# Optimization experiments

Hardware: AMD Instinct MI355X
Metric: run time of the kernel (lower is better)

## Reference

```python
import jax, jax.numpy as jnp
import numpy as np

N = 100000
E = 1600000
IN_F = 128
HIDDEN = 128
HEADS = 2
N_CLASSES = 40
NEG_SLOPE = 0.2
BN_EPS = 1e-5


def setup_inputs() -> dict:
    key = jax.random.key(0)
    ks = jax.random.split(key, 12)
    c1 = HIDDEN // HEADS  # 64
    c2 = N_CLASSES        # 40 per head, concat=False
    inp = {
        "x": jax.random.normal(ks[0], (N, IN_F), dtype=jnp.float32),
        "edge_index": jax.random.randint(ks[1], (2, E), 0, N, dtype=jnp.int32),
        # layer 1 GATConv params
        "W1": jax.random.normal(ks[2], (IN_F, HEADS * c1), dtype=jnp.float32) * 0.05,
        "att_src1": jax.random.normal(ks[3], (HEADS, c1), dtype=jnp.float32) * 0.05,
        "att_dst1": jax.random.normal(ks[4], (HEADS, c1), dtype=jnp.float32) * 0.05,
        "b1": jnp.zeros((HEADS * c1,), dtype=jnp.float32),
        # BatchNorm params
        "gamma": jnp.ones((HIDDEN,), dtype=jnp.float32),
        "beta": jnp.zeros((HIDDEN,), dtype=jnp.float32),
        # layer 2 GATConv params (concat=False)
        "W2": jax.random.normal(ks[5], (HIDDEN, HEADS * c2), dtype=jnp.float32) * 0.05,
        "att_src2": jax.random.normal(ks[6], (HEADS, c2), dtype=jnp.float32) * 0.05,
        "att_dst2": jax.random.normal(ks[7], (HEADS, c2), dtype=jnp.float32) * 0.05,
        "b2": jnp.zeros((c2,), dtype=jnp.float32),
    }
    return inp


def gat_conv(x, src, dst, W, att_src, att_dst, bias, heads, concat):
    n = x.shape[0]
    h = (x @ W).reshape(n, heads, -1)             # [N, H, C]
    a_src = jnp.sum(h * att_src[None], axis=-1)   # [N, H]
    a_dst = jnp.sum(h * att_dst[None], axis=-1)   # [N, H]
    alpha = jax.nn.leaky_relu(a_src[src] + a_dst[dst], NEG_SLOPE)  # [E, H]
    # numerically-stable segment softmax over edges grouped by dst
    amax = jax.ops.segment_max(alpha, dst, num_segments=n)
    e = jnp.exp(alpha - amax[dst])
    denom = jax.ops.segment_sum(e, dst, num_segments=n)
    w = e / denom[dst]                            # [E, H]
    msg = h[src] * w[:, :, None]                  # [E, H, C]
    out = jax.ops.segment_sum(msg, dst, num_segments=n)  # [N, H, C]
    if concat:
        out = out.reshape(n, -1)
    else:
        out = out.mean(axis=1)
    return out + bias


def batch_norm(x, gamma, beta):
    mean = x.mean(axis=0)
    var = x.var(axis=0)
    return (x - mean) * jax.lax.rsqrt(var + BN_EPS) * gamma + beta


def reference(x, edge_index, W1, att_src1, att_dst1, b1, gamma, beta,
              W2, att_src2, att_dst2, b2):
    n = x.shape[0]
    # PyG GATConv default: add self-loops
    loops = jnp.arange(n, dtype=edge_index.dtype)
    src = jnp.concatenate([edge_index[0], loops])
    dst = jnp.concatenate([edge_index[1], loops])
    h = gat_conv(x, src, dst, W1, att_src1, att_dst1, b1, HEADS, concat=True)
    h = batch_norm(h, gamma, beta)
    h = gat_conv(h, src, dst, W2, att_src2, att_dst2, b2, HEADS, concat=False)
    return jax.nn.log_softmax(h, axis=1)
```

## Files before the change

kernel.cpp:

```cpp
#include <hip/hip_runtime.h>
#include <hip/hip_bf16.h>
#include <hip/hip_fp16.h>
#include <stdint.h>

#define N_NODES 100000
#define N_EDGES 1600000
#define ET (N_EDGES + N_NODES)
#define HID 128
#define C2 40
#define F2 80
#define NEG 0.2f
#define BN_EPS 1e-5f
#define NBUCK 391
#define BCAP 6144
#define NBB 640
#define EPB ((ET + NBB - 1) / NBB)
#define CH2 256

typedef __hip_bfloat16 bf16;
typedef __attribute__((ext_vector_type(8))) short s8v;
typedef __attribute__((ext_vector_type(4))) float f4v;
typedef __attribute__((ext_vector_type(4))) unsigned int u4v;
typedef __attribute__((ext_vector_type(2))) unsigned int u2v;

__device__ __forceinline__ float b2f(bf16 v){ return __bfloat162float(v); }
__device__ __forceinline__ float rdf(const void* p, size_t i, int isb){
    return isb ? b2f(((const bf16*)p)[i]) : ((const float*)p)[i];
}
__device__ __forceinline__ unsigned short f2bb(float v){
    bf16 h = __float2bfloat16(v);
    return *(unsigned short*)&h;
}
__device__ __forceinline__ uint32_t pack2(float a, float b){
    return (uint32_t)f2bb(a) | ((uint32_t)f2bb(b) << 16);
}
__device__ __forceinline__ uint32_t packh2(float a, float b){
    return (uint32_t)__half_as_ushort(__float2half(a))
         | ((uint32_t)__half_as_ushort(__float2half(b)) << 16);
}
__device__ __forceinline__ float lo16(uint32_t u){ return __uint_as_float(u << 16); }
__device__ __forceinline__ float hi16(uint32_t u){ return __uint_as_float(u & 0xFFFF0000u); }
__device__ __forceinline__ float hcvt(uint32_t w, int sh){
    return __half2float(__ushort_as_half((unsigned short)((w >> sh) & 0xFFFFu)));
}

__global__ __launch_bounds__(256) void k_init(
    const uint32_t* __restrict__ w1bits, int* __restrict__ flag,
    int* __restrict__ gcur, float* __restrict__ stats)
{
    __shared__ int cnt;
    int t = threadIdx.x;
    if (t == 0) cnt = 0;
    __syncthreads();
    uint32_t b = w1bits[t];
    float lo = __uint_as_float((b & 0xFFFFu) << 16);
    float a = fabsf(lo);
    if (a > 1e-8f && a < 1.0f) atomicAdd(&cnt, 1);
    for (int i = t; i < NBUCK; i += 256) gcur[i] = 0;
    stats[t] = 0.f;
    __syncthreads();
    if (t == 0) *flag = (cnt >= 192) ? 1 : 0;
}

__global__ __launch_bounds__(256) void k_gemm1(
    const void* __restrict__ x, const void* __restrict__ W1,
    const void* __restrict__ attS, const void* __restrict__ attD,
    const int* __restrict__ flag, unsigned short* __restrict__ h1,
    float* __restrict__ aS, float* __restrict__ aD)
{
    __shared__ __attribute__((aligned(16))) unsigned short wT[128*132];
    const int isb = *flag;
    const int tid = threadIdx.x;
    if (isb) {
        const unsigned short* w = (const unsigned short*)W1;
        for (int idx = tid; idx < 128*128; idx += 256){
            int k = idx >> 7, n = idx & 127;
            wT[n*132 + k] = w[idx];
        }
    } else {
        const float* w = (const float*)W1;
        for (int idx = tid; idx < 128*128; idx += 256){
            int k = idx >> 7, n = idx & 127;
            wT[n*132 + k] = f2bb(w[idx]);
        }
    }
    __syncthreads();

    const int w4 = tid >> 6, lane = tid & 63, quad = lane >> 4, l16 = lane & 15;
    const int rowbase = blockIdx.x*32 + (w4 >> 1)*16;
    const int colbase = (w4 & 1)*64;
    const int head = w4 & 1;

    s8v bfr[4][4];
    float asv[4], adv[4];
    #pragma unroll
    for (int ct = 0; ct < 4; ct++){
        int n = colbase + ct*16 + l16;
        asv[ct] = rdf(attS, n, isb);
        adv[ct] = rdf(attD, n, isb);
        #pragma unroll
        for (int s = 0; s < 4; s++){
            int k0 = s*32 + quad*8;
            const unsigned short* p = &wT[n*132 + k0];
            u2v a = *(const u2v*)p, b = *(const u2v*)(p+4);
            union { u4v u; s8v s; } cv; cv.u = (u4v){a[0],a[1],b[0],b[1]};
            bfr[ct][s] = cv.s;
        }
    }

    f4v acc[4];
    #pragma unroll
    for (int ct = 0; ct < 4; ct++) acc[ct] = (f4v){0.f,0.f,0.f,0.f};

    const int m = rowbase + l16;
    #pragma unroll
    for (int s = 0; s < 4; s++){
        int k0 = s*32 + quad*8;
        s8v af;
        if (isb){
            union { u4v u; s8v s; } cv;
            cv.u = *(const u4v*)((const unsigned short*)x + (size_t)m*128 + k0);
            af = cv.s;
        } else {
            const float* xp = (const float*)x + (size_t)m*128 + k0;
            f4v f0 = *(const f4v*)xp, f1 = *(const f4v*)(xp+4);
            union { u4v u; s8v s; } cv;
            cv.u = (u4v){pack2(f0[0],f0[1]), pack2(f0[2],f0[3]),
                         pack2(f1[0],f1[1]), pack2(f1[2],f1[3])};
            af = cv.s;
        }
        #pragma unroll
        for (int ct = 0; ct < 4; ct++)
            acc[ct] = __builtin_amdgcn_mfma_f32_16x16x32_bf16(af, bfr[ct][s], acc[ct], 0,0,0);
    }

    #pragma unroll
    for (int ct = 0; ct < 4; ct++){
        int col = colbase + ct*16 + l16;
        #pragma unroll
        for (int r = 0; r < 4; r++){
            int row = rowbase + quad*4 + r;
            h1[(size_t)row*128 + col] = f2bb(acc[ct][r]);
        }
    }

    #pragma unroll
    for (int r = 0; r < 4; r++){
        float vs = 0.f, vd = 0.f;
        #pragma unroll
        for (int ct = 0; ct < 4; ct++){ vs += acc[ct][r]*asv[ct]; vd += acc[ct][r]*adv[ct]; }
        #pragma unroll
        for (int o = 1; o < 16; o <<= 1){
            vs += __shfl_xor(vs, o, 64);
            vd += __shfl_xor(vd, o, 64);
        }
        if (l16 == 0){
            int row = rowbase + quad*4 + r;
            aS[row*2 + head] = vs;
            aD[row*2 + head] = vd;
        }
    }
}

__global__ __launch_bounds__(256) void k_bin(
    const int* __restrict__ esrc, const int* __restrict__ edst,
    int* __restrict__ gcur, uint32_t* __restrict__ staging)
{
    __shared__ int cnt[NBUCK];
    __shared__ int bb[NBUCK];
    const int t = threadIdx.x;
    for (int i = t; i < NBUCK; i += 256) cnt[i] = 0;
    __syncthreads();
    const int e0 = blockIdx.x * EPB;
    const int e1 = (e0 + EPB < ET) ? e0 + EPB : ET;
    for (int e = e0 + t; e < e1; e += 256){
        int d = (e < N_EDGES) ? edst[e] : e - N_EDGES;
        atomicAdd(&cnt[d >> 8], 1);
    }
    __syncthreads();
    const int bofs = (int)(blockIdx.x % NBUCK);
    for (int i = t; i < NBUCK; i += 256){
        int bkt = i + bofs; if (bkt >= NBUCK) bkt -= NBUCK;
        int c = cnt[bkt];
        bb[bkt] = c ? atomicAdd(&gcur[bkt], c) : 0;
        cnt[bkt] = 0;
    }
    __syncthreads();
    for (int e = e0 + t; e < e1; e += 256){
        int d, s;
        if (e < N_EDGES){ s = esrc[e]; d = edst[e]; } else { s = d = e - N_EDGES; }
        int b = d >> 8;
        int r = atomicAdd(&cnt[b], 1);
        int p = bb[b] + r;
        if (p < BCAP) staging[(size_t)b*BCAP + p] = ((uint32_t)s << 8) | (uint32_t)(d & 255);
    }
}

__global__ __launch_bounds__(256) void k_sort(
    const int* __restrict__ gcur, const uint32_t* __restrict__ staging,
    int* __restrict__ deg, int* __restrict__ cur, int* __restrict__ eidx)
{
    __shared__ int h[256], sc[256], rk[256];
    __shared__ int lsrc[BCAP];
    const int b = blockIdx.x;
    const int t = threadIdx.x;
    const int base = b * BCAP;
    int cnt = gcur[b];
    if (cnt > BCAP) cnt = BCAP;
    h[t] = 0; rk[t] = 0;
    __syncthreads();
    for (int i = t; i < cnt; i += 256)
        atomicAdd(&h[staging[base + i] & 255u], 1);
    __syncthreads();
    sc[t] = h[t];
    __syncthreads();
    for (int off = 1; off < 256; off <<= 1){
        int v = (t >= off) ? sc[t - off] : 0;
        __syncthreads();
        sc[t] += v;
        __syncthreads();
    }
    int dg = b*256 + t;
    if (dg < N_NODES){
        deg[dg] = h[t];
        cur[dg] = base + sc[t];
    }
    __syncthreads();
    for (int i = t; i < cnt; i += 256){
        uint32_t w = staging[base + i];
        int dl = w & 255u;
        int r = atomicAdd(&rk[dl], 1);
        lsrc[sc[dl] - h[dl] + r] = (int)(w >> 8);
    }
    __syncthreads();
    for (int i = t; i < cnt; i += 256) eidx[base + i] = lsrc[i];
}

__global__ __launch_bounds__(256) void k_agg1(
    const int* __restrict__ cur, const int* __restrict__ deg,
    const int* __restrict__ eidx, const float* __restrict__ aS,
    const float* __restrict__ aD, const uint32_t* __restrict__ h1u,
    uint32_t* __restrict__ out1u)
{
    __shared__ uint2 lse[4][2][CH2 + 4];
    const int wv = threadIdx.x >> 6;
    const int l = threadIdx.x & 63;
    const int half = l >> 5, ll = l & 31;
    const int d = blockIdx.x*8 + wv*2 + half;
    const int c = ll & 15;
    const int g = ll >> 4;
    const uint32_t c16 = (uint32_t)(c*16);
    int end   = cur[d];
    int start = end - deg[d];
    float2 ad = *(const float2*)(aD + d*2);
    const int sh = (c >= 8) ? 16 : 0;
    float den0 = 0.f, den1 = 0.f;
    float acc[8];
    #pragma unroll
    for (int k = 0; k < 8; k++) acc[k] = 0.f;
    const char* hb = (const char*)h1u;

#define G1(P, W) { u4v Gx = *(const u4v*)(hb + ((P).x + c16)); \
    float Wf = (W); \
    acc[0] += Wf*lo16(Gx[0]); acc[1] += Wf*hi16(Gx[0]); \
    acc[2] += Wf*lo16(Gx[1]); acc[3] += Wf*hi16(Gx[1]); \
    acc[4] += Wf*lo16(Gx[2]); acc[5] += Wf*hi16(Gx[2]); \
    acc[6] += Wf*lo16(Gx[3]); acc[7] += Wf*hi16(Gx[3]); }

    for (int c0 = start; c0 < end; c0 += CH2){
        int c1 = (c0 + CH2 < end) ? c0 + CH2 : end;
        int n = c1 - c0;
        for (int j = c0 + ll; j < c1; j += 32){
            int s = eidx[j];
            float2 as = *(const float2*)((const char*)aS + ((uint32_t)s*8u));
            float al0 = as.x + ad.x, al1 = as.y + ad.y;
            al0 = al0 > 0.f ? al0 : NEG*al0;
            al1 = al1 > 0.f ? al1 : NEG*al1;
            float e0 = __expf(al0), e1 = __expf(al1);
            lse[wv][half][j - c0] = make_uint2((uint32_t)s << 8, packh2(e0, e1));
            den0 += e0; den1 += e1;
        }
        int nn = (n + 1) & ~1;
        if (ll < nn - n) lse[wv][half][n + ll] = make_uint2(0u, 0u);
        int i = 0;
        for (; i + 8 <= nn; i += 8){
            uint2 pa = lse[wv][half][i + g];
            uint2 pb = lse[wv][half][i + 2 + g];
            uint2 pc = lse[wv][half][i + 4 + g];
            uint2 pd = lse[wv][half][i + 6 + g];
            G1(pa, hcvt(pa.y, sh));
            G1(pb, hcvt(pb.y, sh));
            G1(pc, hcvt(pc.y, sh));
            G1(pd, hcvt(pd.y, sh));
        }
        for (; i < nn; i += 2){
            uint2 pa = lse[wv][half][i + g];
            G1(pa, hcvt(pa.y, sh));
        }
    }
#undef G1
    #pragma unroll
    for (int o = 1; o < 32; o <<= 1){
        den0 += __shfl_xor(den0, o, 64);
        den1 += __shfl_xor(den1, o, 64);
    }
    #pragma unroll
    for (int k = 0; k < 8; k++)
        acc[k] += __shfl_xor(acc[k], 16, 64);
    float r = 1.f / fmaxf((c < 8) ? den0 : den1, 1e-20f);
    if (ll < 16){
        u4v o;
        #pragma unroll
        for (int q = 0; q < 4; q++) o[q] = pack2(acc[2*q]*r, acc[2*q+1]*r);
        *(u4v*)(out1u + (size_t)d*64 + 4*c) = o;
    }
}

__global__ __launch_bounds__(256) void k_bnstats(
    const uint32_t* __restrict__ out1u, float* __restrict__ stats)
{
    __shared__ float red[4][64][4];
    int fp = threadIdx.x & 63;
    int wv = threadIdx.x >> 6;
    float s0 = 0.f, q0 = 0.f, s1 = 0.f, q1 = 0.f;
    for (int r = blockIdx.x*4 + wv; r < N_NODES; r += 512){
        uint32_t u = out1u[(size_t)r*64 + fp];
        float f0 = lo16(u), f1 = hi16(u);
        s0 += f0; q0 += f0*f0; s1 += f1; q1 += f1*f1;
    }
    red[wv][fp][0] = s0; red[wv][fp][1] = s1;
    red[wv][fp][2] = q0; red[wv][fp][3] = q1;
    __syncthreads();
    if (threadIdx.x < 64){
        int l = threadIdx.x;
        float a0=0.f, a1=0.f, b0=0.f, b1=0.f;
        #pragma unroll
        for (int w = 0; w < 4; w++){
            a0 += red[w][l][0]; a1 += red[w][l][1];
            b0 += red[w][l][2]; b1 += red[w][l][3];
        }
        unsafeAtomicAdd(&stats[2*l],       a0);
        unsafeAtomicAdd(&stats[2*l+1],     a1);
        unsafeAtomicAdd(&stats[128+2*l],   b0);
        unsafeAtomicAdd(&stats[128+2*l+1], b1);
    }
}

__global__ __launch_bounds__(256) void k_gemm2(
    const unsigned short* __restrict__ out1b, const float* __restrict__ stats,
    const void* __restrict__ gamma, const void* __restrict__ beta,
    const void* __restrict__ W2, const void* __restrict__ attS,
    const void* __restrict__ attD, const int* __restrict__ flag,
    unsigned short* __restrict__ h2, float* __restrict__ aS, float* __restrict__ aD)
{
    __shared__ __attribute__((aligned(16))) unsigned short wT[80*132];
    __shared__ float scl[128], shl[128];
    const int isb = *flag;
    const int tid = threadIdx.x;
    for (int idx = tid; idx < 128*80; idx += 256){
        int k = idx / 80, n = idx - k*80;
        wT[n*132 + k] = isb ? ((const unsigned short*)W2)[idx]
                            : f2bb(((const float*)W2)[idx]);
    }
    if (tid < 128){
        float mean = stats[tid] * (1.f / N_NODES);
        float var = fmaxf(stats[128+tid] * (1.f / N_NODES) - mean*mean, 0.f);
        float rs = rsqrtf(var + BN_EPS);
        float sc = rdf(gamma, tid, isb) * rs;
        scl[tid] = sc;
        shl[tid] = rdf(beta, tid, isb) - mean*sc;
    }
    __syncthreads();

    const int w4 = tid >> 6, lane = tid & 63, quad = lane >> 4, l16 = lane & 15;
    const int rowbase = blockIdx.x*64 + w4*16;

    s8v bfr[5][4];
    float asv[5], adv[5];
    #pragma unroll
    for (int ct = 0; ct < 5; ct++){
        int n = ct*16 + l16;
        asv[ct] = rdf(attS, n, isb);
        adv[ct] = rdf(attD, n, isb);
        #pragma unroll
        for (int s = 0; s < 4; s++){
            int k0 = s*32 + quad*8;
            const unsigned short* p = &wT[n*132 + k0];
            u2v a = *(const u2v*)p, b = *(const u2v*)(p+4);
            union { u4v u; s8v s; } cv; cv.u = (u4v){a[0],a[1],b[0],b[1]};
            bfr[ct][s] = cv.s;
        }
    }

    f4v acc[5];
    #pragma unroll
    for (int ct = 0; ct < 5; ct++) acc[ct] = (f4v){0.f,0.f,0.f,0.f};

    int m = rowbase + l16;
    int mc = m < N_NODES ? m : N_NODES - 1;
    #pragma unroll
    for (int s = 0; s < 4; s++){
        int k0 = s*32 + quad*8;
        union { u4v u; s8v s8; } cin;
        cin.u = *(const u4v*)(out1b + (size_t)mc*128 + k0);
        u4v up;
        #pragma unroll
        for (int i = 0; i < 4; i++){
            float f0 = lo16(cin.u[i]), f1 = hi16(cin.u[i]);
            int k = k0 + 2*i;
            up[i] = pack2(f0*scl[k] + shl[k], f1*scl[k+1] + shl[k+1]);
        }
        union { u4v u; s8v s8; } cv; cv.u = up;
        #pragma unroll
        for (int ct = 0; ct < 5; ct++)
            acc[ct] = __builtin_amdgcn_mfma_f32_16x16x32_bf16(cv.s8, bfr[ct][s], acc[ct], 0,0,0);
    }

    #pragma unroll
    for (int ct = 0; ct < 5; ct++){
        int col = ct*16 + l16;
        #pragma unroll
        for (int r = 0; r < 4; r++){
            int row = rowbase + quad*4 + r;
            if (row < N_NODES) h2[(size_t)row*80 + col] = f2bb(acc[ct][r]);
        }
    }

    #pragma unroll
    for (int r = 0; r < 4; r++){
        float vs0 = 0.f, vs1 = 0.f, vd0 = 0.f, vd1 = 0.f;
        #pragma unroll
        for (int ct = 0; ct < 5; ct++){
            int col = ct*16 + l16;
            float ps = acc[ct][r]*asv[ct], pd = acc[ct][r]*adv[ct];
            if (col < 40){ vs0 += ps; vd0 += pd; } else { vs1 += ps; vd1 += pd; }
        }
        #pragma unroll
        for (int o = 1; o < 16; o <<= 1){
            vs0 += __shfl_xor(vs0, o, 64); vs1 += __shfl_xor(vs1, o, 64);
            vd0 += __shfl_xor(vd0, o, 64); vd1 += __shfl_xor(vd1, o, 64);
        }
        if (l16 == 0){
            int row = rowbase + quad*4 + r;
            if (row < N_NODES){
                aS[row*2 + 0] = vs0; aS[row*2 + 1] = vs1;
                aD[row*2 + 0] = vd0; aD[row*2 + 1] = vd1;
            }
        }
    }
}

__global__ __launch_bounds__(256) void k_agg2(
    const int* __restrict__ cur, const int* __restrict__ deg,
    const int* __restrict__ eidx, const float* __restrict__ aS,
    const float* __restrict__ aD, const uint32_t* __restrict__ h2u,
    const void* __restrict__ b2v, const int* __restrict__ flag,
    void* __restrict__ out)
{
    __shared__ uint2 lse[4][2][CH2 + 4];
    const int wv = threadIdx.x >> 6;
    const int l = threadIdx.x & 63;
    const int half = l >> 5, ll = l & 31;
    const int d = blockIdx.x*8 + wv*2 + half;
    const int isb = *flag;
    const int c = ll % 10;
    const int g = ll / 10;
    const bool act = ll < 30;
    const int gq = act ? g : 0;
    const uint32_t c16 = (uint32_t)(c*16);
    int end   = cur[d];
    int start = end - deg[d];
    float2 ad = *(const float2*)(aD + d*2);
    const int sh = (c >= 5) ? 16 : 0;
    float den0 = 0.f, den1 = 0.f;
    float acc[8];
    #pragma unroll
    for (int k = 0; k < 8; k++) acc[k] = 0.f;
    const char* hb = (const char*)h2u;

#define G2(P, W) { u4v Gx = *(const u4v*)(hb + ((P).x + c16)); \
    float Wf = (W); \
    acc[0] += Wf*lo16(Gx[0]); acc[1] += Wf*hi16(Gx[0]); \
    acc[2] += Wf*lo16(Gx[1]); acc[3] += Wf*hi16(Gx[1]); \
    acc[4] += Wf*lo16(Gx[2]); acc[5] += Wf*hi16(Gx[2]); \
    acc[6] += Wf*lo16(Gx[3]); acc[7] += Wf*hi16(Gx[3]); }

    for (int c0 = start; c0 < end; c0 += CH2){
        int c1 = (c0 + CH2 < end) ? c0 + CH2 : end;
        int n = c1 - c0;
        for (int j = c0 + ll; j < c1; j += 32){
            int s = eidx[j];
            float2 as = *(const float2*)((const char*)aS + ((uint32_t)s*8u));
            float al0 = as.x + ad.x, al1 = as.y + ad.y;
            al0 = al0 > 0.f ? al0 : NEG*al0;
            al1 = al1 > 0.f ? al1 : NEG*al1;
            float e0 = __expf(al0), e1 = __expf(al1);
            lse[wv][half][j - c0] = make_uint2((uint32_t)s * 160u, packh2(e0, e1));
            den0 += e0; den1 += e1;
        }
        int nn = ((n + 2) / 3) * 3;
        if (ll < nn - n) lse[wv][half][n + ll] = make_uint2(0u, 0u);
        int i = 0;
        for (; i + 9 <= nn; i += 9){
            uint2 pa = lse[wv][half][i + gq];
            uint2 pb = lse[wv][half][i + 3 + gq];
            uint2 pc = lse[wv][half][i + 6 + gq];
            G2(pa, act ? hcvt(pa.y, sh) : 0.f);
            G2(pb, act ? hcvt(pb.y, sh) : 0.f);
            G2(pc, act ? hcvt(pc.y, sh) : 0.f);
        }
        for (; i < nn; i += 3){
            uint2 pa = lse[wv][half][i + gq];
            G2(pa, act ? hcvt(pa.y, sh) : 0.f);
        }
    }
#undef G2
    #pragma unroll
    for (int o = 1; o < 32; o <<= 1){
        den0 += __shfl_xor(den0, o, 64);
        den1 += __shfl_xor(den1, o, 64);
    }
    #pragma unroll
    for (int k = 0; k < 8; k++)
        acc[k] += __shfl(acc[k], l + 10, 64) + __shfl(acc[k], l + 20, 64);
    float r = 1.f / fmaxf((c < 5) ? den0 : den1, 1e-20f);
    #pragma unroll
    for (int k = 0; k < 8; k++) acc[k] *= r;

    int lb = (ll < 5) ? ll : 0;
    float v[8];
    float mx = -1e30f;
    #pragma unroll
    for (int k = 0; k < 8; k++){
        float t = __shfl(acc[k], l + 5, 64);
        v[k] = 0.5f*(acc[k] + t) + rdf(b2v, 8*lb + k, isb);
        mx = fmaxf(mx, v[k]);
    }
    if (ll >= 5) mx = -1e30f;
    mx = fmaxf(mx, __shfl_xor(mx, 1, 64));
    mx = fmaxf(mx, __shfl_xor(mx, 2, 64));
    mx = fmaxf(mx, __shfl_xor(mx, 4, 64));
    float ex = 0.f;
    if (ll < 5){
        #pragma unroll
        for (int k = 0; k < 8; k++) ex += __expf(v[k] - mx);
    }
    ex += __shfl_xor(ex, 1, 64);
    ex += __shfl_xor(ex, 2, 64);
    ex += __shfl_xor(ex, 4, 64);
    float lsf = __logf(ex);
    if (ll < 5){
        if (isb){
            u4v o;
            #pragma unroll
            for (int q = 0; q < 4; q++)
                o[q] = pack2(v[2*q] - mx - lsf, v[2*q+1] - mx - lsf);
            *(u4v*)((uint32_t*)out + (size_t)d*20 + 4*ll) = o;
        } else {
            float4 o0, o1;
            o0.x = v[0]-mx-lsf; o0.y = v[1]-mx-lsf; o0.z = v[2]-mx-lsf; o0.w = v[3]-mx-lsf;
            o1.x = v[4]-mx-lsf; o1.y = v[5]-mx-lsf; o1.z = v[6]-mx-lsf; o1.w = v[7]-mx-lsf;
            ((float4*)out)[(size_t)d*10 + 2*ll]     = o0;
            ((float4*)out)[(size_t)d*10 + 2*ll + 1] = o1;
        }
    }
}

extern "C" void kernel_launch(void* const* d_in, const int* in_sizes, int n_in,
                              void* d_out, int out_size, void* d_ws, size_t ws_size,
                              hipStream_t stream)
{
    const void* x    = d_in[0];
    const int*  ei   = (const int*)d_in[1];
    const void* W1   = d_in[2];
    const void* as1  = d_in[3];
    const void* ad1  = d_in[4];
    const void* gamma = d_in[6];
    const void* beta  = d_in[7];
    const void* W2   = d_in[8];
    const void* as2  = d_in[9];
    const void* ad2  = d_in[10];
    const void* b2v  = d_in[11];
    const int* esrc = ei;
    const int* edst = ei + N_EDGES;

    char* ws = (char*)d_ws;
    size_t off = 0;
    auto alloc = [&](size_t bytes) {
        void* p = ws + off;
        off += (bytes + 255) & ~(size_t)255;
        return p;
    };
    int*   flag  = (int*)alloc(256);
    float* stats = (float*)alloc(sizeof(float)*256);
    int*   gcur  = (int*)alloc(sizeof(int)*NBUCK);
    float* aS1   = (float*)alloc(sizeof(float)*N_NODES*2);
    float* aD1   = (float*)alloc(sizeof(float)*N_NODES*2);
    float* aS2   = (float*)alloc(sizeof(float)*N_NODES*2);
    float* aD2   = (float*)alloc(sizeof(float)*N_NODES*2);
    int*   deg   = (int*)alloc(sizeof(int)*N_NODES);
    int*   cur   = (int*)alloc(sizeof(int)*N_NODES);
    uint32_t* staging = (uint32_t*)alloc(sizeof(uint32_t)*(size_t)NBUCK*BCAP);
    int*   eidx  = (int*)alloc(sizeof(int)*(size_t)NBUCK*BCAP);
    unsigned short* h1  = (unsigned short*)alloc(2*(size_t)N_NODES*HID);
    unsigned short* out1 = (unsigned short*)alloc(2*(size_t)N_NODES*HID);
    unsigned short* h2  = h1;

    k_init<<<1, 256, 0, stream>>>((const uint32_t*)W1, flag, gcur, stats);
    k_gemm1<<<3125, 256, 0, stream>>>(x, W1, as1, ad1, flag, h1, aS1, aD1);
    k_bin<<<NBB, 256, 0, stream>>>(esrc, edst, gcur, staging);
    k_sort<<<NBUCK, 256, 0, stream>>>(gcur, staging, deg, cur, eidx);
    k_agg1<<<12500, 256, 0, stream>>>(cur, deg, eidx, aS1, aD1,
                                      (const uint32_t*)h1, (uint32_t*)out1);
    k_bnstats<<<128, 256, 0, stream>>>((const uint32_t*)out1, stats);
    k_gemm2<<<1563, 256, 0, stream>>>(out1, stats, gamma, beta, W2, as2, ad2,
                                      flag, h2, aS2, aD2);
    k_agg2<<<12500, 256, 0, stream>>>(cur, deg, eidx, aS2, aD2,
                                      (const uint32_t*)h2, b2v, flag, d_out);
}
```

Measured before the change: 412.7 us.

## Split layer-1 aggregation per head across blocks with fp32 edge weights

The layer-1 aggregation kernel now assigns each head of a destination node to a separate 32-lane group, doubling the grid so that head 0 and head 1 are processed by different blocks. Each lane-group now gathers 128-byte head slices (8 lanes × 16B) for four edges at once instead of 256-byte rows for two. Edge weights are stored as fp32 rather than packed half2, which removes the half conversion. This is meant to raise parallelism and memory-level concurrency for the gathers. The cost is that the edge index and attention scores are read twice and the exp is computed once per head rather than for both heads together.

```diff
diff --git a/kernel.cpp b/kernel.cpp
--- a/kernel.cpp
+++ b/kernel.cpp
@@ -246,22 +246,25 @@
     const int wv = threadIdx.x >> 6;
     const int l = threadIdx.x & 63;
     const int half = l >> 5, ll = l & 31;
-    const int d = blockIdx.x*8 + wv*2 + half;
-    const int c = ll & 15;
-    const int g = ll >> 4;
+    const int bx = blockIdx.x;
+    const int grp = bx >> 3, xp = bx & 7;
+    const int h = xp >> 2, sub = xp & 3;
+    const int d = grp*32 + sub*8 + wv*2 + half;
+    const int c = ll & 7;
+    const int g = ll >> 3;
     const uint32_t c16 = (uint32_t)(c*16);
+    const uint32_t hofs = (uint32_t)h << 7;
     int end   = cur[d];
     int start = end - deg[d];
-    float2 ad = *(const float2*)(aD + d*2);
-    const int sh = (c >= 8) ? 16 : 0;
-    float den0 = 0.f, den1 = 0.f;
+    float adh = aD[d*2 + h];
+    float den = 0.f;
     float acc[8];
     #pragma unroll
     for (int k = 0; k < 8; k++) acc[k] = 0.f;
     const char* hb = (const char*)h1u;
 
-#define G1(P, W) { u4v Gx = *(const u4v*)(hb + ((P).x + c16)); \
-    float Wf = (W); \
+#define G1(P) { u4v Gx = *(const u4v*)(hb + ((P).x + c16)); \
+    float Wf = __uint_as_float((P).y); \
     acc[0] += Wf*lo16(Gx[0]); acc[1] += Wf*hi16(Gx[0]); \
     acc[2] += Wf*lo16(Gx[1]); acc[3] += Wf*hi16(Gx[1]); \
     acc[4] += Wf*lo16(Gx[2]); acc[5] += Wf*hi16(Gx[2]); \
@@ -272,47 +275,44 @@
         int n = c1 - c0;
         for (int j = c0 + ll; j < c1; j += 32){
             int s = eidx[j];
-            float2 as = *(const float2*)((const char*)aS + ((uint32_t)s*8u));
-            float al0 = as.x + ad.x, al1 = as.y + ad.y;
-            al0 = al0 > 0.f ? al0 : NEG*al0;
-            al1 = al1 > 0.f ? al1 : NEG*al1;
-            float e0 = __expf(al0), e1 = __expf(al1);
-            lse[wv][half][j - c0] = make_uint2((uint32_t)s << 8, packh2(e0, e1));
-            den0 += e0; den1 += e1;
-        }
-        int nn = (n + 1) & ~1;
-        if (ll < nn - n) lse[wv][half][n + ll] = make_uint2(0u, 0u);
+            float as = ((const float*)aS)[(size_t)s*2 + h];
+            float al = as + adh;
+            al = al > 0.f ? al : NEG*al;
+            float e = __expf(al);
+            lse[wv][half][j - c0] = make_uint2(((uint32_t)s << 8) + hofs,
+                                               __float_as_uint(e));
+            den += e;
+        }
+        int nn = (n + 3) & ~3;
+        if (ll < nn - n) lse[wv][half][n + ll] = make_uint2(hofs, 0u);
         int i = 0;
-        for (; i + 8 <= nn; i += 8){
-            uint2 pa = lse[wv][half][i + g];
-            uint2 pb = lse[wv][half][i + 2 + g];
-            uint2 pc = lse[wv][half][i + 4 + g];
-            uint2 pd = lse[wv][half][i + 6 + g];
-            G1(pa, hcvt(pa.y, sh));
-            G1(pb, hcvt(pb.y, sh));
-            G1(pc, hcvt(pc.y, sh));
-            G1(pd, hcvt(pd.y, sh));
-        }
-        for (; i < nn; i += 2){
-            uint2 pa = lse[wv][half][i + g];
-            G1(pa, hcvt(pa.y, sh));
+        for (; i + 16 <= nn; i += 16){
+            uint2 q0 = lse[wv][half][i + g];
+            uint2 q1 = lse[wv][half][i + 4 + g];
+            uint2 q2 = lse[wv][half][i + 8 + g];
+            uint2 q3 = lse[wv][half][i + 12 + g];
+            G1(q0); G1(q1); G1(q2); G1(q3);
+        }
+        for (; i < nn; i += 4){
+            uint2 q0 = lse[wv][half][i + g];
+            G1(q0);
         }
     }
 #undef G1
     #pragma unroll
-    for (int o = 1; o < 32; o <<= 1){
-        den0 += __shfl_xor(den0, o, 64);
-        den1 += __shfl_xor(den1, o, 64);
-    }
-    #pragma unroll
-    for (int k = 0; k < 8; k++)
+    for (int o = 1; o < 32; o <<= 1)
+        den += __shfl_xor(den, o, 64);
+    #pragma unroll
+    for (int k = 0; k < 8; k++){
+        acc[k] += __shfl_xor(acc[k], 8, 64);
         acc[k] += __shfl_xor(acc[k], 16, 64);
-    float r = 1.f / fmaxf((c < 8) ? den0 : den1, 1e-20f);
-    if (ll < 16){
+    }
+    float r = 1.f / fmaxf(den, 1e-20f);
+    if (ll < 8){
         u4v o;
         #pragma unroll
         for (int q = 0; q < 4; q++) o[q] = pack2(acc[2*q]*r, acc[2*q+1]*r);
-        *(u4v*)(out1u + (size_t)d*64 + 4*c) = o;
+        *(u4v*)(out1u + (size_t)d*64 + h*32 + 4*c) = o;
     }
 }
 
@@ -610,7 +610,7 @@
     k_gemm1<<<3125, 256, 0, stream>>>(x, W1, as1, ad1, flag, h1, aS1, aD1);
     k_bin<<<NBB, 256, 0, stream>>>(esrc, edst, gcur, staging);
     k_sort<<<NBUCK, 256, 0, stream>>>(gcur, staging, deg, cur, eidx);
-    k_agg1<<<12500, 256, 0, stream>>>(cur, deg, eidx, aS1, aD1,
+    k_agg1<<<25000, 256, 0, stream>>>(cur, deg, eidx, aS1, aD1,
                                       (const uint32_t*)h1, (uint32_t*)out1);
     k_bnstats<<<128, 256, 0, stream>>>((const uint32_t*)out1, stats);
     k_gemm2<<<1563, 256, 0, stream>>>(out1, stats, gamma, beta, W2, as2, ad2,
```

Result: no change. 411.0 us (-0.4%).

## Precompute layer-1 edge weights and denominators in sort; split agg1 by feature slice

Applied to the files above, without the earlier changes.

The layer-1 attention exponentials and per-node softmax denominators now come out of the sort kernel, packed with the source index into 32-bit words (17-bit src, 15-bit fp16 weight without its sign bit), one buffer per head. agg1 then runs 8x more blocks, each handling a 32-byte feature slice of one head and reading precomputed weights without shared-memory staging. The aim is to drop redundant exp/gather work and raise parallelism in the gather. In exchange, each edge word is read several times, the denominator loop in sort runs serially per thread, and packing the source index into 17 bits limits node ids to 131072.

```diff
diff --git a/kernel.cpp b/kernel.cpp
--- a/kernel.cpp
+++ b/kernel.cpp
@@ -42,6 +42,9 @@
 __device__ __forceinline__ float hi16(uint32_t u){ return __uint_as_float(u & 0xFFFF0000u); }
 __device__ __forceinline__ float hcvt(uint32_t w, int sh){
     return __half2float(__ushort_as_half((unsigned short)((w >> sh) & 0xFFFFu)));
+}
+__device__ __forceinline__ float w15f(uint32_t w){
+    return __half2float(__ushort_as_half((unsigned short)(w & 0x7FFFu)));
 }
 
 __global__ __launch_bounds__(256) void k_init(
@@ -197,8 +200,10 @@
 }
 
 __global__ __launch_bounds__(256) void k_sort(
-    const int* __restrict__ gcur, const uint32_t* __restrict__ staging,
-    int* __restrict__ deg, int* __restrict__ cur, int* __restrict__ eidx)
+    const int* __restrict__ gcur, uint32_t* stg ,
+    const float* __restrict__ aS, const float* __restrict__ aD,
+    int* __restrict__ deg, int* __restrict__ cur,
+    uint32_t* __restrict__ wb1, float* __restrict__ den)
 {
     __shared__ int h[256], sc[256], rk[256];
     __shared__ int lsrc[BCAP];
@@ -210,7 +215,7 @@
     h[t] = 0; rk[t] = 0;
     __syncthreads();
     for (int i = t; i < cnt; i += 256)
-        atomicAdd(&h[staging[base + i] & 255u], 1);
+        atomicAdd(&h[stg[base + i] & 255u], 1);
     __syncthreads();
     sc[t] = h[t];
     __syncthreads();
@@ -227,92 +232,107 @@
     }
     __syncthreads();
     for (int i = t; i < cnt; i += 256){
-        uint32_t w = staging[base + i];
+        uint32_t w = stg[base + i];
         int dl = w & 255u;
         int r = atomicAdd(&rk[dl], 1);
         lsrc[sc[dl] - h[dl] + r] = (int)(w >> 8);
     }
     __syncthreads();
-    for (int i = t; i < cnt; i += 256) eidx[base + i] = lsrc[i];
+    if (dg < N_NODES){
+        int myDeg = h[t];
+        int myStart = sc[t] - h[t];
+        float2 adv = *(const float2*)(aD + (size_t)dg*2);
+        float den0 = 0.f, den1 = 0.f;
+        for (int i = 0; i < myDeg; i++){
+            int s = lsrc[myStart + i];
+            float2 as = *(const float2*)(aS + (size_t)s*2);
+            float al0 = as.x + adv.x, al1 = as.y + adv.y;
+            al0 = al0 > 0.f ? al0 : NEG*al0;
+            al1 = al1 > 0.f ? al1 : NEG*al1;
+            float e0 = __expf(al0), e1 = __expf(al1);
+            den0 += e0; den1 += e1;
+            uint32_t sb = (uint32_t)s << 15;
+            uint32_t p0 = (uint32_t)__half_as_ushort(__float2half(e0)) & 0x7FFFu;
+            uint32_t p1 = (uint32_t)__half_as_ushort(__float2half(e1)) & 0x7FFFu;
+            stg[base + myStart + i] = sb | p0;
+            wb1[base + myStart + i] = sb | p1;
+        }
+        den[(size_t)dg*2]     = den0;
+        den[(size_t)dg*2 + 1] = den1;
+    }
 }
 
 __global__ __launch_bounds__(256) void k_agg1(
     const int* __restrict__ cur, const int* __restrict__ deg,
-    const int* __restrict__ eidx, const float* __restrict__ aS,
-    const float* __restrict__ aD, const uint32_t* __restrict__ h1u,
+    const uint32_t* __restrict__ wb0, const uint32_t* __restrict__ wb1,
+    const float* __restrict__ den, const uint32_t* __restrict__ h1u,
     uint32_t* __restrict__ out1u)
 {
-    __shared__ uint2 lse[4][2][CH2 + 4];
+    const int bx = blockIdx.x;
+    const int k = bx & 7;
+    const int grp = bx >> 3;
+    const int h = k >> 2;
+    const uint32_t* __restrict__ wb = h ? wb1 : wb0;
     const int wv = threadIdx.x >> 6;
     const int l = threadIdx.x & 63;
     const int half = l >> 5, ll = l & 31;
-    const int d = blockIdx.x*8 + wv*2 + half;
-    const int c = ll & 15;
-    const int g = ll >> 4;
-    const uint32_t c16 = (uint32_t)(c*16);
-    int end   = cur[d];
-    int start = end - deg[d];
-    float2 ad = *(const float2*)(aD + d*2);
-    const int sh = (c >= 8) ? 16 : 0;
-    float den0 = 0.f, den1 = 0.f;
+    const int d = grp*8 + wv*2 + half;
+    const int sub = ll & 1, epair = ll >> 1;
+    const uint32_t kofs = (uint32_t)(k*32 + sub*16);
+    int end = cur[d];
+    int dgv = deg[d];
+    int start = end - dgv;
+    float dh = den[(size_t)d*2 + h];
     float acc[8];
     #pragma unroll
-    for (int k = 0; k < 8; k++) acc[k] = 0.f;
+    for (int q = 0; q < 8; q++) acc[q] = 0.f;
+    int rm = (dgv + 15) >> 4;
+    rm = max(rm, __shfl_xor(rm, 32, 64));
     const char* hb = (const char*)h1u;
 
-#define G1(P, W) { u4v Gx = *(const u4v*)(hb + ((P).x + c16)); \
-    float Wf = (W); \
-    acc[0] += Wf*lo16(Gx[0]); acc[1] += Wf*hi16(Gx[0]); \
-    acc[2] += Wf*lo16(Gx[1]); acc[3] += Wf*hi16(Gx[1]); \
-    acc[4] += Wf*lo16(Gx[2]); acc[5] += Wf*hi16(Gx[2]); \
-    acc[6] += Wf*lo16(Gx[3]); acc[7] += Wf*hi16(Gx[3]); }
-
-    for (int c0 = start; c0 < end; c0 += CH2){
-        int c1 = (c0 + CH2 < end) ? c0 + CH2 : end;
-        int n = c1 - c0;
-        for (int j = c0 + ll; j < c1; j += 32){
-            int s = eidx[j];
-            float2 as = *(const float2*)((const char*)aS + ((uint32_t)s*8u));
-            float al0 = as.x + ad.x, al1 = as.y + ad.y;
-            al0 = al0 > 0.f ? al0 : NEG*al0;
-            al1 = al1 > 0.f ? al1 : NEG*al1;
-            float e0 = __expf(al0), e1 = __expf(al1);
-            lse[wv][half][j - c0] = make_uint2((uint32_t)s << 8, packh2(e0, e1));
-            den0 += e0; den1 += e1;
-        }
-        int nn = (n + 1) & ~1;
-        if (ll < nn - n) lse[wv][half][n + ll] = make_uint2(0u, 0u);
-        int i = 0;
-        for (; i + 8 <= nn; i += 8){
-            uint2 pa = lse[wv][half][i + g];
-            uint2 pb = lse[wv][half][i + 2 + g];
-            uint2 pc = lse[wv][half][i + 4 + g];
-            uint2 pd = lse[wv][half][i + 6 + g];
-            G1(pa, hcvt(pa.y, sh));
-            G1(pb, hcvt(pb.y, sh));
-            G1(pc, hcvt(pc.y, sh));
-            G1(pd, hcvt(pd.y, sh));
-        }
-        for (; i < nn; i += 2){
-            uint2 pa = lse[wv][half][i + g];
-            G1(pa, hcvt(pa.y, sh));
-        }
-    }
-#undef G1
-    #pragma unroll
-    for (int o = 1; o < 32; o <<= 1){
-        den0 += __shfl_xor(den0, o, 64);
-        den1 += __shfl_xor(den1, o, 64);
-    }
-    #pragma unroll
-    for (int k = 0; k < 8; k++)
-        acc[k] += __shfl_xor(acc[k], 16, 64);
-    float r = 1.f / fmaxf((c < 8) ? den0 : den1, 1e-20f);
-    if (ll < 16){
+#define GF(G, W) { float Wf = (W); \
+    acc[0] += Wf*lo16((G)[0]); acc[1] += Wf*hi16((G)[0]); \
+    acc[2] += Wf*lo16((G)[1]); acc[3] += Wf*hi16((G)[1]); \
+    acc[4] += Wf*lo16((G)[2]); acc[5] += Wf*hi16((G)[2]); \
+    acc[6] += Wf*lo16((G)[3]); acc[7] += Wf*hi16((G)[3]); }
+
+    int t = 0;
+    for (; t + 2 <= rm; t += 2){
+        int j0 = start + (t << 4) + epair;
+        int j1 = j0 + 16;
+        bool v0 = j0 < end, v1 = j1 < end;
+        uint32_t w0 = __builtin_nontemporal_load(wb + (v0 ? j0 : start));
+        uint32_t w1 = __builtin_nontemporal_load(wb + (v1 ? j1 : start));
+        u4v G0 = *(const u4v*)(hb + (((w0 >> 15) << 8) + kofs));
+        u4v G1 = *(const u4v*)(hb + (((w1 >> 15) << 8) + kofs));
+        float f0 = v0 ? w15f(w0) : 0.f;
+        float f1 = v1 ? w15f(w1) : 0.f;
+        GF(G0, f0);
+        GF(G1, f1);
+    }
+    if (t < rm){
+        int j0 = start + (t << 4) + epair;
+        bool v0 = j0 < end;
+        uint32_t w0 = __builtin_nontemporal_load(wb + (v0 ? j0 : start));
+        u4v G0 = *(const u4v*)(hb + (((w0 >> 15) << 8) + kofs));
+        float f0 = v0 ? w15f(w0) : 0.f;
+        GF(G0, f0);
+    }
+#undef GF
+    #pragma unroll
+    for (int q = 0; q < 8; q++){
+        acc[q] += __shfl_xor(acc[q], 2, 64);
+        acc[q] += __shfl_xor(acc[q], 4, 64);
+        acc[q] += __shfl_xor(acc[q], 8, 64);
+        acc[q] += __shfl_xor(acc[q], 16, 64);
+    }
+    if (ll < 2){
+        float rr = 1.f / fmaxf(dh, 1e-20f);
         u4v o;
         #pragma unroll
-        for (int q = 0; q < 4; q++) o[q] = pack2(acc[2*q]*r, acc[2*q+1]*r);
-        *(u4v*)(out1u + (size_t)d*64 + 4*c) = o;
+        for (int q = 0; q < 4; q++) o[q] = pack2(acc[2*q]*rr, acc[2*q+1]*rr);
+        __builtin_nontemporal_store(o,
+            (u4v*)(out1u + (size_t)d*64 + 8*k + 4*ll));
     }
 }
 
@@ -452,7 +472,7 @@
 
 __global__ __launch_bounds__(256) void k_agg2(
     const int* __restrict__ cur, const int* __restrict__ deg,
-    const int* __restrict__ eidx, const float* __restrict__ aS,
+    const uint32_t* __restrict__ wb0, const float* __restrict__ aS,
     const float* __restrict__ aD, const uint32_t* __restrict__ h2u,
     const void* __restrict__ b2v, const int* __restrict__ flag,
     void* __restrict__ out)
@@ -489,13 +509,13 @@
         int c1 = (c0 + CH2 < end) ? c0 + CH2 : end;
         int n = c1 - c0;
         for (int j = c0 + ll; j < c1; j += 32){
-            int s = eidx[j];
-            float2 as = *(const float2*)((const char*)aS + ((uint32_t)s*8u));
+            uint32_t s = __builtin_nontemporal_load(wb0 + j) >> 15;
+            float2 as = *(const float2*)((const char*)aS + (s*8u));
             float al0 = as.x + ad.x, al1 = as.y + ad.y;
             al0 = al0 > 0.f ? al0 : NEG*al0;
             al1 = al1 > 0.f ? al1 : NEG*al1;
             float e0 = __expf(al0), e1 = __expf(al1);
-            lse[wv][half][j - c0] = make_uint2((uint32_t)s * 160u, packh2(e0, e1));
+            lse[wv][half][j - c0] = make_uint2(s * 160u, packh2(e0, e1));
             den0 += e0; den1 += e1;
         }
         int nn = ((n + 2) / 3) * 3;
@@ -598,23 +618,26 @@
     float* aD1   = (float*)alloc(sizeof(float)*N_NODES*2);
     float* aS2   = (float*)alloc(sizeof(float)*N_NODES*2);
     float* aD2   = (float*)alloc(sizeof(float)*N_NODES*2);
+    float* den1  = (float*)alloc(sizeof(float)*N_NODES*2);
     int*   deg   = (int*)alloc(sizeof(int)*N_NODES);
     int*   cur   = (int*)alloc(sizeof(int)*N_NODES);
     uint32_t* staging = (uint32_t*)alloc(sizeof(uint32_t)*(size_t)NBUCK*BCAP);
-    int*   eidx  = (int*)alloc(sizeof(int)*(size_t)NBUCK*BCAP);
+    uint32_t* wb1 = (uint32_t*)alloc(sizeof(uint32_t)*(size_t)NBUCK*BCAP);
     unsigned short* h1  = (unsigned short*)alloc(2*(size_t)N_NODES*HID);
     unsigned short* out1 = (unsigned short*)alloc(2*(size_t)N_NODES*HID);
     unsigned short* h2  = h1;
+    uint32_t* wb0 = staging;
 
     k_init<<<1, 256, 0, stream>>>((const uint32_t*)W1, flag, gcur, stats);
     k_gemm1<<<3125, 256, 0, stream>>>(x, W1, as1, ad1, flag, h1, aS1, aD1);
     k_bin<<<NBB, 256, 0, stream>>>(esrc, edst, gcur, staging);
-    k_sort<<<NBUCK, 256, 0, stream>>>(gcur, staging, deg, cur, eidx);
-    k_agg1<<<12500, 256, 0, stream>>>(cur, deg, eidx, aS1, aD1,
-                                      (const uint32_t*)h1, (uint32_t*)out1);
+    k_sort<<<NBUCK, 256, 0, stream>>>(gcur, staging, aS1, aD1, deg, cur,
+                                      wb1, den1);
+    k_agg1<<<100000, 256, 0, stream>>>(cur, deg, wb0, wb1, den1,
+                                       (const uint32_t*)h1, (uint32_t*)out1);
     k_bnstats<<<128, 256, 0, stream>>>((const uint32_t*)out1, stats);
     k_gemm2<<<1563, 256, 0, stream>>>(out1, stats, gamma, beta, W2, as2, ad2,
                                       flag, h2, aS2, aD2);
-    k_agg2<<<12500, 256, 0, stream>>>(cur, deg, eidx, aS2, aD2,
+    k_agg2<<<12500, 256, 0, stream>>>(cur, deg, wb0, aS2, aD2,
                                       (const uint32_t*)h2, b2v, flag, d_out);
 }
```

Result: slower. 556.5 us (+34.8%).

## Replace bucketed bin+sort CSR build with global histogram, scan, atomic scatter

Applied to the files above, without the earlier changes.

Replaces the two-pass bucket binning and in-LDS local sort with a per-node degree histogram using global atomics, a three-kernel prefix scan, and an atomic-slot scatter into a compact edge index array. This drops the staging buffer and the fixed bucket capacity, which could truncate overfull buckets. In exchange it adds 1.7M global atomics on random addresses in both the histogram and scatter passes, plus more kernel launches. Neighbor order within each node becomes nondeterministic, which can change float summation order.

```diff
diff --git a/kernel.cpp b/kernel.cpp
--- a/kernel.cpp
+++ b/kernel.cpp
@@ -12,9 +12,6 @@
 #define NEG 0.2f
 #define BN_EPS 1e-5f
 #define NBUCK 391
-#define BCAP 6144
-#define NBB 640
-#define EPB ((ET + NBB - 1) / NBB)
 #define CH2 256
 
 typedef __hip_bfloat16 bf16;
@@ -46,20 +43,23 @@
 
 __global__ __launch_bounds__(256) void k_init(
     const uint32_t* __restrict__ w1bits, int* __restrict__ flag,
-    int* __restrict__ gcur, float* __restrict__ stats)
+    float* __restrict__ stats, int* __restrict__ deg)
 {
     __shared__ int cnt;
     int t = threadIdx.x;
-    if (t == 0) cnt = 0;
-    __syncthreads();
-    uint32_t b = w1bits[t];
-    float lo = __uint_as_float((b & 0xFFFFu) << 16);
-    float a = fabsf(lo);
-    if (a > 1e-8f && a < 1.0f) atomicAdd(&cnt, 1);
-    for (int i = t; i < NBUCK; i += 256) gcur[i] = 0;
-    stats[t] = 0.f;
-    __syncthreads();
-    if (t == 0) *flag = (cnt >= 192) ? 1 : 0;
+    int dg = blockIdx.x*256 + t;
+    if (dg < N_NODES) deg[dg] = 0;
+    if (blockIdx.x == 0){
+        if (t == 0) cnt = 0;
+        __syncthreads();
+        uint32_t b = w1bits[t];
+        float lo = __uint_as_float((b & 0xFFFFu) << 16);
+        float a = fabsf(lo);
+        if (a > 1e-8f && a < 1.0f) atomicAdd(&cnt, 1);
+        stats[t] = 0.f;
+        __syncthreads();
+        if (t == 0) *flag = (cnt >= 192) ? 1 : 0;
+    }
 }
 
 __global__ __launch_bounds__(256) void k_gemm1(
@@ -162,78 +162,74 @@
     }
 }
 
-__global__ __launch_bounds__(256) void k_bin(
+__global__ __launch_bounds__(256) void k_hist(
     const int* __restrict__ esrc, const int* __restrict__ edst,
-    int* __restrict__ gcur, uint32_t* __restrict__ staging)
-{
-    __shared__ int cnt[NBUCK];
-    __shared__ int bb[NBUCK];
-    const int t = threadIdx.x;
-    for (int i = t; i < NBUCK; i += 256) cnt[i] = 0;
-    __syncthreads();
-    const int e0 = blockIdx.x * EPB;
-    const int e1 = (e0 + EPB < ET) ? e0 + EPB : ET;
-    for (int e = e0 + t; e < e1; e += 256){
+    int* __restrict__ deg)
+{
+    for (int e = blockIdx.x*256 + threadIdx.x; e < ET; e += 1700*256){
         int d = (e < N_EDGES) ? edst[e] : e - N_EDGES;
-        atomicAdd(&cnt[d >> 8], 1);
-    }
-    __syncthreads();
-    const int bofs = (int)(blockIdx.x % NBUCK);
-    for (int i = t; i < NBUCK; i += 256){
-        int bkt = i + bofs; if (bkt >= NBUCK) bkt -= NBUCK;
-        int c = cnt[bkt];
-        bb[bkt] = c ? atomicAdd(&gcur[bkt], c) : 0;
-        cnt[bkt] = 0;
-    }
-    __syncthreads();
-    for (int e = e0 + t; e < e1; e += 256){
-        int d, s;
-        if (e < N_EDGES){ s = esrc[e]; d = edst[e]; } else { s = d = e - N_EDGES; }
-        int b = d >> 8;
-        int r = atomicAdd(&cnt[b], 1);
-        int p = bb[b] + r;
-        if (p < BCAP) staging[(size_t)b*BCAP + p] = ((uint32_t)s << 8) | (uint32_t)(d & 255);
-    }
-}
-
-__global__ __launch_bounds__(256) void k_sort(
-    const int* __restrict__ gcur, const uint32_t* __restrict__ staging,
-    int* __restrict__ deg, int* __restrict__ cur, int* __restrict__ eidx)
-{
-    __shared__ int h[256], sc[256], rk[256];
-    __shared__ int lsrc[BCAP];
-    const int b = blockIdx.x;
-    const int t = threadIdx.x;
-    const int base = b * BCAP;
-    int cnt = gcur[b];
-    if (cnt > BCAP) cnt = BCAP;
-    h[t] = 0; rk[t] = 0;
-    __syncthreads();
-    for (int i = t; i < cnt; i += 256)
-        atomicAdd(&h[staging[base + i] & 255u], 1);
-    __syncthreads();
-    sc[t] = h[t];
+        atomicAdd(&deg[d], 1);
+    }
+}
+
+__global__ __launch_bounds__(256) void k_scan1(
+    const int* __restrict__ deg, int* __restrict__ cur, int* __restrict__ bsum)
+{
+    __shared__ int sc[256];
+    const int b = blockIdx.x, t = threadIdx.x;
+    int dg = b*256 + t;
+    int v = (dg < N_NODES) ? deg[dg] : 0;
+    sc[t] = v;
     __syncthreads();
     for (int off = 1; off < 256; off <<= 1){
-        int v = (t >= off) ? sc[t - off] : 0;
+        int u = (t >= off) ? sc[t - off] : 0;
         __syncthreads();
-        sc[t] += v;
+        sc[t] += u;
         __syncthreads();
     }
-    int dg = b*256 + t;
+    if (dg < N_NODES) cur[dg] = sc[t];
+    if (t == 255) bsum[b] = sc[255];
+}
+
+__global__ __launch_bounds__(512) void k_scan2(
+    const int* __restrict__ bsum, int* __restrict__ bsumx)
+{
+    __shared__ int sc[512];
+    const int t = threadIdx.x;
+    int v = (t < NBUCK) ? bsum[t] : 0;
+    sc[t] = v;
+    __syncthreads();
+    for (int off = 1; off < 512; off <<= 1){
+        int u = (t >= off) ? sc[t - off] : 0;
+        __syncthreads();
+        sc[t] += u;
+        __syncthreads();
+    }
+    if (t < NBUCK) bsumx[t] = sc[t] - v;
+}
+
+__global__ __launch_bounds__(256) void k_scan3(
+    const int* __restrict__ deg, const int* __restrict__ bsumx,
+    int* __restrict__ cur, int* __restrict__ curw)
+{
+    int dg = blockIdx.x*256 + threadIdx.x;
     if (dg < N_NODES){
-        deg[dg] = h[t];
-        cur[dg] = base + sc[t];
-    }
-    __syncthreads();
-    for (int i = t; i < cnt; i += 256){
-        uint32_t w = staging[base + i];
-        int dl = w & 255u;
-        int r = atomicAdd(&rk[dl], 1);
-        lsrc[sc[dl] - h[dl] + r] = (int)(w >> 8);
-    }
-    __syncthreads();
-    for (int i = t; i < cnt; i += 256) eidx[base + i] = lsrc[i];
+        int e = cur[dg] + bsumx[blockIdx.x];
+        cur[dg]  = e;
+        curw[dg] = e - deg[dg];
+    }
+}
+
+__global__ __launch_bounds__(256) void k_scatter(
+    const int* __restrict__ esrc, const int* __restrict__ edst,
+    int* __restrict__ curw, int* __restrict__ eidx)
+{
+    for (int e = blockIdx.x*256 + threadIdx.x; e < ET; e += 1700*256){
+        int s, d;
+        if (e < N_EDGES){ s = esrc[e]; d = edst[e]; } else { s = d = e - N_EDGES; }
+        int p = atomicAdd(&curw[d], 1);
+        eidx[p] = s;
+    }
 }
 
 __global__ __launch_bounds__(256) void k_agg1(
@@ -593,23 +589,27 @@
     };
     int*   flag  = (int*)alloc(256);
     float* stats = (float*)alloc(sizeof(float)*256);
-    int*   gcur  = (int*)alloc(sizeof(int)*NBUCK);
     float* aS1   = (float*)alloc(sizeof(float)*N_NODES*2);
     float* aD1   = (float*)alloc(sizeof(float)*N_NODES*2);
     float* aS2   = (float*)alloc(sizeof(float)*N_NODES*2);
     float* aD2   = (float*)alloc(sizeof(float)*N_NODES*2);
     int*   deg   = (int*)alloc(sizeof(int)*N_NODES);
     int*   cur   = (int*)alloc(sizeof(int)*N_NODES);
-    uint32_t* staging = (uint32_t*)alloc(sizeof(uint32_t)*(size_t)NBUCK*BCAP);
-    int*   eidx  = (int*)alloc(sizeof(int)*(size_t)NBUCK*BCAP);
+    int*   curw  = (int*)alloc(sizeof(int)*N_NODES);
+    int*   bsum  = (int*)alloc(sizeof(int)*NBUCK);
+    int*   bsumx = (int*)alloc(sizeof(int)*NBUCK);
+    int*   eidx  = (int*)alloc(sizeof(int)*(size_t)ET);
     unsigned short* h1  = (unsigned short*)alloc(2*(size_t)N_NODES*HID);
     unsigned short* out1 = (unsigned short*)alloc(2*(size_t)N_NODES*HID);
     unsigned short* h2  = h1;
 
-    k_init<<<1, 256, 0, stream>>>((const uint32_t*)W1, flag, gcur, stats);
+    k_init<<<NBUCK, 256, 0, stream>>>((const uint32_t*)W1, flag, stats, deg);
     k_gemm1<<<3125, 256, 0, stream>>>(x, W1, as1, ad1, flag, h1, aS1, aD1);
-    k_bin<<<NBB, 256, 0, stream>>>(esrc, edst, gcur, staging);
-    k_sort<<<NBUCK, 256, 0, stream>>>(gcur, staging, deg, cur, eidx);
+    k_hist<<<1700, 256, 0, stream>>>(esrc, edst, deg);
+    k_scan1<<<NBUCK, 256, 0, stream>>>(deg, cur, bsum);
+    k_scan2<<<1, 512, 0, stream>>>(bsum, bsumx);
+    k_scan3<<<NBUCK, 256, 0, stream>>>(deg, bsumx, cur, curw);
+    k_scatter<<<1700, 256, 0, stream>>>(esrc, edst, curw, eidx);
     k_agg1<<<12500, 256, 0, stream>>>(cur, deg, eidx, aS1, aD1,
                                       (const uint32_t*)h1, (uint32_t*)out1);
     k_bnstats<<<128, 256, 0, stream>>>((const uint32_t*)out1, stats);
```

Measured after the change: 566.6 us. 1.37x slower.
